# Kernel optimization log

Measured on AMD Instinct MI355X. Metric: run time of the kernel, lower is better.

Reference implementation:

```python
import jax, jax.numpy as jnp
import numpy as np
import math

K = 1.0          # Lorentz curvature parameter (points satisfy -t^2 + |s|^2 = -K)
SQRT_K = 1.0
HEADS = 8
HEAD_DIM = 64
EPS_LN = 1e-5


def add_time(xs):
    # lift space vector onto the hyperboloid: t = sqrt(|s|^2 + K)
    t = jnp.sqrt(jnp.sum(xs * xs, axis=-1, keepdims=True) + K)
    return jnp.concatenate([t, xs], axis=-1)


def logmap0(x):
    t, s = x[..., :1], x[..., 1:]
    d = SQRT_K * jnp.arccosh(jnp.maximum(t / SQRT_K, 1.0))
    sn = jnp.maximum(jnp.linalg.norm(s, axis=-1, keepdims=True), 1e-8)
    return jnp.concatenate([jnp.zeros_like(t), d * s / sn], axis=-1)


def expmap0(u):
    s = u[..., 1:]
    n = jnp.maximum(jnp.linalg.norm(s, axis=-1, keepdims=True), 1e-8)
    t = SQRT_K * jnp.cosh(n / SQRT_K)
    return jnp.concatenate([t, SQRT_K * jnp.sinh(n / SQRT_K) * s / n], axis=-1)


def lorentz_ln(x, g, b):
    # LayerNorm on space coords, then recompute time
    s = x[..., 1:]
    mu = jnp.mean(s, axis=-1, keepdims=True)
    var = jnp.var(s, axis=-1, keepdims=True)
    s = (s - mu) / jnp.sqrt(var + EPS_LN) * g + b
    return add_time(s)


def lfc(x, W, activation=None):
    # LorentzFullyConnected: linear on full input -> space coords, recompute time
    s = x @ W.T
    if activation is not None:
        s = activation(s)
    return add_time(s)


def lfc_heads(x, W):
    b, n, _ = x.shape
    s = (x @ W.T).reshape(b, n, HEADS, HEAD_DIM).transpose(0, 2, 1, 3)
    return add_time(s)  # (b, h, n, head_dim+1), per-head time coordinate


def _mha_haa(x, Wq, Wk, Wv, Wo, temperature, beta_raw, tau_raw, lambda_raw):
    q = lfc_heads(x, Wq)
    k = lfc_heads(x, Wk)
    v = lfc_heads(x, Wv)
    q_t, k_t = q[..., :1], k[..., :1]
    q_s, k_s = q[..., 1:], k[..., 1:]
    # Lorentz inner product <q,k>_L = -t_q t_k + <s_q, s_k>, shape (b,h,n,n)
    inner_QK = -q_t @ jnp.swapaxes(k_t, -1, -2) + q_s @ jnp.swapaxes(k_s, -1, -2)
    inner_OQ = -SQRT_K * q_t                       # (b,h,n,1)
    inner_OK = -SQRT_K * jnp.swapaxes(k_t, -1, -2)  # (b,h,1,n)
    norm_sq_QK = jnp.maximum(inner_QK ** 2 / K - K, 0.0)
    norm_sq_OQ = jnp.maximum(inner_OQ ** 2 / K - K, 0.0)
    numer_Z = inner_OK + inner_QK * inner_OQ / K
    denom_Z = jnp.sqrt(norm_sq_QK * norm_sq_OQ + 0.005 ** 2)
    Z = jnp.clip(numer_Z / denom_Z, -1.0, 1.0)
    c_tilde = jnp.arccosh(jnp.maximum(q_t / SQRT_K, 1.0 + 0.001))
    beta = jax.nn.softplus(beta_raw)
    B = jnp.sqrt(jax.nn.relu(1.0 - (beta / jnp.sinh(c_tilde)) ** 2) + 1e-8)
    lam = jax.nn.softplus(lambda_raw)
    dist_raw = SQRT_K * jnp.arccosh(jnp.maximum(-inner_QK / K, 1.0 + 0.001))
    d_soft = 40.0 * jnp.tanh(dist_raw / 40.0)
    sd = d_soft / 15.0
    H = sd + jax.nn.softplus(-2.0 * sd) - math.log(2.0)
    tau = jax.nn.softplus(tau_raw)
    m = 0.1
    Phi = jax.nn.softplus(B + Z - m) - math.log(1.0 + math.exp(-m))
    score = jax.nn.softmax((-lam * H - tau * Phi) / temperature, axis=-1)
    # Lorentz expmap aggregation: weighted mean in tangent space at origin
    v_tan = logmap0(v)
    mean_tan = (score @ v_tan) / (jnp.sum(score, axis=-1, keepdims=True) + 1e-8)
    attn = expmap0(mean_tan).transpose(0, 2, 1, 3)  # (b,n,h,head_dim+1)
    b_, n_ = attn.shape[:2]
    a_s = attn[..., 1:].reshape(b_, n_, -1)   # (b,n,h*head_dim)
    a_t = attn[..., :1].reshape(b_, n_, -1)   # (b,n,h)
    t2 = jnp.sum(a_t ** 2, axis=-1, keepdims=True) - (HEADS - 1) * K
    attn = jnp.concatenate([jnp.sqrt(jnp.maximum(t2, 1e-8)), a_s], axis=-1)
    return lfc(attn, Wo)


def reference(x, Wq, Wk, Wv, Wo, W1, W2, ln1_g, ln1_b, ln2_g, ln2_b,
              temperature, beta_raw, tau_raw, lambda_raw):
    out = _mha_haa(lorentz_ln(x, ln1_g, ln1_b), Wq, Wk, Wv, Wo,
                   temperature, beta_raw, tau_raw, lambda_raw)
    out_s = out[..., 1:] + x[..., 1:]                 # residual on space coords
    y = lorentz_ln(add_time(out_s), ln2_g, ln2_b)
    h = lfc(y, W1, activation=lambda z: jax.nn.gelu(z, approximate=False))
    h = lfc(h, W2)
    out_s = h[..., 1:] + out_s
    return add_time(out_s)


def setup_inputs() -> dict:
    key = jax.random.key(0)
    ks = jax.random.split(key, 8)
    B, N, D = 2, 1024, 513
    xs = 0.5 * jax.random.normal(ks[0], (B, N, D - 1), dtype=jnp.float32)
    x = add_time(xs)
    sc = 1.0 / math.sqrt(D)
    return {
        "x": x,
        "Wq": sc * jax.random.normal(ks[1], (512, 513), dtype=jnp.float32),
        "Wk": sc * jax.random.normal(ks[2], (512, 513), dtype=jnp.float32),
        "Wv": sc * jax.random.normal(ks[3], (512, 513), dtype=jnp.float32),
        "Wo": sc * jax.random.normal(ks[4], (512, 513), dtype=jnp.float32),
        "W1": sc * jax.random.normal(ks[5], (2048, 513), dtype=jnp.float32),
        "W2": (1.0 / math.sqrt(2049)) * jax.random.normal(ks[6], (512, 2049), dtype=jnp.float32),
        "ln1_g": jnp.ones((512,), jnp.float32),
        "ln1_b": jnp.zeros((512,), jnp.float32),
        "ln2_g": jnp.ones((512,), jnp.float32),
        "ln2_b": jnp.zeros((512,), jnp.float32),
        "temperature": jnp.ones((1,), jnp.float32),
        "beta_raw": jnp.full((1,), math.log(math.e - 1.0), jnp.float32),
        "tau_raw": jnp.full((1,), math.log(math.exp(0.1) - 1.0), jnp.float32),
        "lambda_raw": jnp.full((1,), math.log(math.e - 1.0), jnp.float32),
    }
```

## Files before the change

### kernel.cpp

```cpp
#include <hip/hip_runtime.h>
#include <math.h>

#define DEV static __device__ __forceinline__

typedef __bf16 bf16_t;
typedef __bf16 bf16x8 __attribute__((ext_vector_type(8)));
typedef float f32x4 __attribute__((ext_vector_type(4)));

#define MFMA16(a,b,c) __builtin_amdgcn_mfma_f32_16x16x32_bf16(a,b,c,0,0,0)

DEV float frcp(float x){ return __builtin_amdgcn_rcpf(x); }
DEV float softplus_fast(float x){
  return fmaxf(x, 0.f) + __logf(1.f + __expf(-fabsf(x)));
}
DEV float tanh_fast(float z){
  float e2 = __expf(2.f * z);
  return (e2 - 1.f) * frcp(e2 + 1.f);
}
DEV float gelu_fast(float v){
  float u = 0.7978845608028654f * fmaf(0.044715f * v, v * v, v);
  u = fminf(fmaxf(u, -15.f), 15.f);
  return 0.5f * v * (1.f + tanh_fast(u));
}

DEV void gl_lds16(const void* g, void* l) {
  __builtin_amdgcn_global_load_lds((const __attribute__((address_space(1))) void*)g,
                                   (__attribute__((address_space(3))) void*)l, 16, 0, 0);
}

DEV float waveReduceSum(float v){
  #pragma unroll
  for (int o = 32; o > 0; o >>= 1) v += __shfl_xor(v, o, 64);
  return v;
}
DEV float blockReduceSum(float v, float* sh){
  v = waveReduceSum(v);
  int w = threadIdx.x >> 6;
  int nw = blockDim.x >> 6;
  __syncthreads();
  if ((threadIdx.x & 63) == 0) sh[w] = v;
  __syncthreads();
  float r = sh[0];
  for (int i = 1; i < nw; i++) r += sh[i];
  return r;
}

DEV int2 xcd_swz(int gx, int gy){
  int id = blockIdx.y * gx + blockIdx.x;
  int q = (gx * gy) >> 3;
  int s = (id & 7) * q + (id >> 3);
  int2 r; r.x = s % gx; r.y = s / gx;
  return r;
}

__global__ __launch_bounds__(256) void prep(
    const float* __restrict__ xin,
    const float* __restrict__ g, const float* __restrict__ b,
    const float* __restrict__ Wq, const float* __restrict__ Wk,
    const float* __restrict__ Wv, const float* __restrict__ Wo,
    const float* __restrict__ W1, const float* __restrict__ W2,
    bf16_t* __restrict__ y, float* __restrict__ ty,
    bf16_t* __restrict__ Wqkvb, bf16_t* __restrict__ Wob,
    bf16_t* __restrict__ W1b, bf16_t* __restrict__ W2b,
    float* __restrict__ wqkv0, float* __restrict__ wo0,
    float* __restrict__ w10, float* __restrict__ w20)
{
  int t = threadIdx.x;
  if (blockIdx.x < 2048) {
    __shared__ float sh[8];
    int row = blockIdx.x;
    const float* xr = xin + (long)row * 513 + 1;
    float a0 = xr[t], a1 = xr[t + 256];
    float s  = blockReduceSum(a0 + a1, sh);
    float s2 = blockReduceSum(a0 * a0 + a1 * a1, sh);
    float mu = s * (1.f / 512.f);
    float var = s2 * (1.f / 512.f) - mu * mu;
    float inv = rsqrtf(var + 1e-5f);
    float y0 = (a0 - mu) * inv * g[t] + b[t];
    float y1v = (a1 - mu) * inv * g[t + 256] + b[t + 256];
    float q = blockReduceSum(y0 * y0 + y1v * y1v, sh);
    bf16_t* yr = y + (long)row * 512;
    yr[t] = (bf16_t)y0;
    yr[t + 256] = (bf16_t)y1v;
    if (t == 0) ty[row] = sqrtf(q + 1.f);
    return;
  }
  long i = (long)(blockIdx.x - 2048) * 256 + t;
  if (i < 786432) {
    long r = i >> 9; int c = (int)(i & 511);
    const float* src = (r < 512) ? Wq + r * 513 : (r < 1024) ? Wk + (r - 512) * 513 : Wv + (r - 1024) * 513;
    Wqkvb[i] = (bf16_t)src[c + 1];
  } else if (i < 1048576) {
    long j = i - 786432;
    long r = j >> 9; int c = (int)(j & 511);
    Wob[j] = (bf16_t)Wo[r * 513 + c + 1];
  } else if (i < 2097152) {
    long j = i - 1048576;
    long r = j >> 9; int c = (int)(j & 511);
    W1b[j] = (bf16_t)W1[r * 513 + c + 1];
  } else if (i < 3145728) {
    long j = i - 2097152;
    long r = j >> 11; int c = (int)(j & 2047);
    W2b[j] = (bf16_t)W2[r * 2049 + c + 1];
  } else if (i < 3150336) {
    int j = (int)(i - 3145728);
    if (j < 1536) {
      wqkv0[j] = (j < 512) ? Wq[(long)j * 513] : (j < 1024) ? Wk[(long)(j - 512) * 513] : Wv[(long)(j - 1024) * 513];
    } else if (j < 2048) wo0[j - 1536] = Wo[(long)(j - 1536) * 513];
    else if (j < 4096)  w10[j - 2048] = W1[(long)(j - 2048) * 513];
    else                w20[j - 4096] = W2[(long)(j - 4096) * 2049];
  }
}

__global__ __launch_bounds__(256) void res_ln(
    const float* __restrict__ woA, const float* __restrict__ woB,
    const float* __restrict__ ch2, const float* __restrict__ wo0,
    const float* __restrict__ xin,
    const float* __restrict__ g, const float* __restrict__ b,
    float* __restrict__ outs,
    bf16_t* __restrict__ y, float* __restrict__ ty)
{
  __shared__ float sh[8];
  int row = blockIdx.x;
  int t = threadIdx.x;
  const float* c = ch2 + (long)row * 8;
  float cs = ((c[0] + c[1]) + (c[2] + c[3])) + ((c[4] + c[5]) + (c[6] + c[7]));
  float tattn = sqrtf(fmaxf(cs - 7.f, 1e-8f));
  long i0 = (long)row * 512 + t, i1 = i0 + 256;
  float a0 = woA[i0] + woB[i0] + tattn * wo0[t]       + xin[(long)row * 513 + 1 + t];
  float a1 = woA[i1] + woB[i1] + tattn * wo0[t + 256] + xin[(long)row * 513 + 1 + t + 256];
  outs[i0] = a0;
  outs[i1] = a1;
  float s  = blockReduceSum(a0 + a1, sh);
  float s2 = blockReduceSum(a0 * a0 + a1 * a1, sh);
  float mu = s * (1.f / 512.f);
  float var = s2 * (1.f / 512.f) - mu * mu;
  float inv = rsqrtf(var + 1e-5f);
  float y0 = (a0 - mu) * inv * g[t] + b[t];
  float y1v = (a1 - mu) * inv * g[t + 256] + b[t + 256];
  float q = blockReduceSum(y0 * y0 + y1v * y1v, sh);
  bf16_t* yr = y + (long)row * 512;
  yr[t] = (bf16_t)y0;
  yr[t + 256] = (bf16_t)y1v;
  if (t == 0) ty[row] = sqrtf(q + 1.f);
}

__global__ __launch_bounds__(256) void final_k(
    const float* __restrict__ hA, const float* __restrict__ hB,
    const float* __restrict__ hC, const float* __restrict__ hD,
    const float* __restrict__ th2p, const float* __restrict__ w20,
    const float* __restrict__ outs,
    float* __restrict__ out)
{
  __shared__ float sh[8];
  int row = blockIdx.x;
  int t = threadIdx.x;
  float p = (t < 32) ? th2p[(long)t * 2048 + row] : 0.f;
  float hn = blockReduceSum(p, sh);
  float th = sqrtf(hn + 1.f);
  long i0 = (long)row * 512 + t, i1 = i0 + 256;
  float o0 = (hA[i0] + hB[i0]) + (hC[i0] + hD[i0]) + th * w20[t]       + outs[i0];
  float o1 = (hA[i1] + hB[i1]) + (hC[i1] + hD[i1]) + th * w20[t + 256] + outs[i1];
  float q = blockReduceSum(o0 * o0 + o1 * o1, sh);
  float* yr = out + (long)row * 513;
  yr[1 + t] = o0;
  yr[1 + t + 256] = o1;
  if (t == 0) yr[0] = sqrtf(q + 1.f);
}

__global__ __launch_bounds__(256) void vtan_tr(
    const bf16_t* __restrict__ qkvsb, bf16_t* __restrict__ VTt)
{
  __shared__ bf16_t tile[64 * 72];
  int z = blockIdx.y, b = z >> 3, h = z & 7;
  int n0 = blockIdx.x * 64;
  int t = threadIdx.x;
  int r = t >> 2, c4 = t & 3;
  const bf16_t* vb = qkvsb + ((long)(b * 1024 + n0 + r) * 1536 + 1024 + h * 64 + c4 * 16);
  bf16x8 v0 = *(const bf16x8*)vb;
  bf16x8 v1 = *(const bf16x8*)(vb + 8);
  float ss = 0.f;
  #pragma unroll
  for (int e = 0; e < 8; e++) {
    float f0 = (float)v0[e], f1 = (float)v1[e];
    ss = fmaf(f0, f0, fmaf(f1, f1, ss));
  }
  ss += __shfl_xor(ss, 1, 64);
  ss += __shfl_xor(ss, 2, 64);
  float vT = sqrtf(1.f + ss);
  float sn0 = sqrtf(ss);
  float coef = __logf(vT + sn0) * frcp(fmaxf(sn0, 1e-8f));
  #pragma unroll
  for (int e = 0; e < 8; e++) {
    tile[(c4 * 16 + e) * 72 + r]     = (bf16_t)(coef * (float)v0[e]);
    tile[(c4 * 16 + 8 + e) * 72 + r] = (bf16_t)(coef * (float)v1[e]);
  }
  __syncthreads();
  int d = t >> 2, cc = (t & 3) * 16;
  bf16x8 o0 = *(const bf16x8*)&tile[d * 72 + cc];
  bf16x8 o1 = *(const bf16x8*)&tile[d * 72 + cc + 8];
  bf16_t* dst = VTt + (long)z * 64 * 1024 + (long)d * 1024 + n0 + cc;
  *(bf16x8*)dst = o0;
  *(bf16x8*)(dst + 8) = o1;
}

__global__ __launch_bounds__(256) void attn_fused(
    const bf16_t* __restrict__ qkvsb,
    const bf16_t* __restrict__ VTt,
    const float* __restrict__ qt, const float* __restrict__ kt,
    const float* __restrict__ Bi,
    bf16_t* __restrict__ attnb,
    float* __restrict__ ch2,
    const float* __restrict__ lam_p, const float* __restrict__ tau_p,
    const float* __restrict__ temp_p)
{
  __shared__ bf16_t Ks[64 * 64];
  __shared__ bf16_t Vs[64 * 64];
  __shared__ bf16_t Ps[32 * 72];
  __shared__ float ot[32 * 65];
  __shared__ float sh_qt[32], sh_Bc[32], sh_kt[64], rs[32];

  const int t = threadIdx.x;
  const int w = t >> 6;
  const int lane = t & 63;
  const int lm = lane & 15, lh = lane >> 4;
  int2 sw = xcd_swz(32, 16);
  const int z = sw.y, b = z >> 3, h = z & 7;
  const int n0 = sw.x * 32;
  const int sb = (((lane & 7) ^ (lane >> 3)) << 4);
  const int r8 = lane >> 3;

  float lam = softplus_fast(lam_p[0]);
  float tau = softplus_fast(tau_p[0]);
  float invT = frcp(temp_p[0]);
  float A1 = -lam * invT, A2 = -tau * invT;
  float A2h = 0.5f * A2, K0 = A2 * 0.048750465f;

  if (t < 32) {
    sh_qt[t] = qt[z * 1024 + n0 + t];
    sh_Bc[t] = Bi[z * 1024 + n0 + t] - 0.1f;
    rs[t] = 0.f;
  }

  const bf16_t* qbase = qkvsb + ((long)(b * 1024 + n0) * 1536 + h * 64);
  gl_lds16((const char*)(qbase + (long)(w * 8 + r8) * 1536) + sb, (char*)Ks + w * 1024);
  __syncthreads();
  bf16x8 qf[2][2];
  #pragma unroll
  for (int i = 0; i < 2; i++)
    #pragma unroll
    for (int kk = 0; kk < 2; kk++)
      qf[i][kk] = *(const bf16x8*)&Ks[(i * 16 + lm) * 64 + (((kk * 4 + lh) ^ (lm & 7)) << 3)];

  f32x4 oacc[2] = {};
  float racc[2][4] = {};

  const bf16_t* kbase = qkvsb + ((long)b * 1024 * 1536 + 512 + h * 64);
  const bf16_t* vbase = VTt + (long)z * 64 * 1024;
  const int sl0 = ((lh) ^ (lm & 7)) << 3;
  const int sl1 = ((4 + lh) ^ (lm & 7)) << 3;

  for (int kv = 0; kv < 16; kv++) {
    __syncthreads();
    {
      const bf16_t* kb = kbase + (long)(kv * 64) * 1536;
      gl_lds16((const char*)(kb + (long)(w * 16 + r8) * 1536) + sb,     (char*)Ks + (w * 2) * 1024);
      gl_lds16((const char*)(kb + (long)(w * 16 + 8 + r8) * 1536) + sb, (char*)Ks + (w * 2 + 1) * 1024);
      const bf16_t* vb = vbase + kv * 64;
      gl_lds16((const char*)(vb + (long)(w * 16 + r8) * 1024) + sb,     (char*)Vs + (w * 2) * 1024);
      gl_lds16((const char*)(vb + (long)(w * 16 + 8 + r8) * 1024) + sb, (char*)Vs + (w * 2 + 1) * 1024);
    }
    if (t < 64) sh_kt[t] = kt[z * 1024 + kv * 64 + t];
    __syncthreads();

    f32x4 sacc[2] = {};
    bf16x8 kf0 = *(const bf16x8*)&Ks[(w * 16 + lm) * 64 + sl0];
    bf16x8 kf1 = *(const bf16x8*)&Ks[(w * 16 + lm) * 64 + sl1];
    sacc[0] = MFMA16(qf[0][0], kf0, sacc[0]);
    sacc[0] = MFMA16(qf[0][1], kf1, sacc[0]);
    sacc[1] = MFMA16(qf[1][0], kf0, sacc[1]);
    sacc[1] = MFMA16(qf[1][1], kf1, sacc[1]);

    float ktv = sh_kt[w * 16 + lm];
    #pragma unroll
    for (int i = 0; i < 2; i++) {
      #pragma unroll
      for (int q = 0; q < 4; q++) {
        int r = i * 16 + lh * 4 + q;
        float qtv = sh_qt[r], Bc = sh_Bc[r];
        float nOQ = fmaf(qtv, qtv, -1.f);
        float inner = fmaf(-qtv, ktv, sacc[i][q]);
        float nQK = fmaxf(fmaf(inner, inner, -1.f), 0.f);
        float ri = __builtin_amdgcn_rsqf(fmaf(nQK, nOQ, 2.5e-5f));
        float zr = fmaf(inner, qtv, ktv) * ri;
        float Zc = fminf(fmaxf(-zr, -1.f), 1.f);
        float xx = fmaxf(-inner, 1.001f);
        float u = fmaf(__log2f(xx), 0.01732868f, 0.01732868f);
        float p = fminf(u * u, 0.09f);
        float H = p * fmaf(p, -6.584f, 3.5556f);
        float a = Zc + Bc;
        float a2 = a * a;
        float lc = a2 * fmaf(a2, fmaf(a2, 0.00034722f, -0.0052083f), 0.125f);
        float lgt = fmaf(A1, H, fmaf(A2, lc, fmaf(A2h, a, K0)));
        float e = __expf(lgt);
        Ps[r * 72 + w * 16 + lm] = (bf16_t)e;
        racc[i][q] += e;
      }
    }
    __syncthreads();

    bf16x8 va0 = *(const bf16x8*)&Vs[(w * 16 + lm) * 64 + sl0];
    bf16x8 va1 = *(const bf16x8*)&Vs[(w * 16 + lm) * 64 + sl1];
    bf16x8 pb00 = *(const bf16x8*)&Ps[lm * 72 + lh * 8];
    bf16x8 pb01 = *(const bf16x8*)&Ps[lm * 72 + 32 + lh * 8];
    bf16x8 pb10 = *(const bf16x8*)&Ps[(16 + lm) * 72 + lh * 8];
    bf16x8 pb11 = *(const bf16x8*)&Ps[(16 + lm) * 72 + 32 + lh * 8];
    oacc[0] = MFMA16(va0, pb00, oacc[0]);
    oacc[0] = MFMA16(va1, pb01, oacc[0]);
    oacc[1] = MFMA16(va0, pb10, oacc[1]);
    oacc[1] = MFMA16(va1, pb11, oacc[1]);
  }

  #pragma unroll
  for (int i = 0; i < 2; i++)
    #pragma unroll
    for (int q = 0; q < 4; q++) {
      float v = racc[i][q];
      v += __shfl_xor(v, 1, 64);
      v += __shfl_xor(v, 2, 64);
      v += __shfl_xor(v, 4, 64);
      v += __shfl_xor(v, 8, 64);
      if (lm == 0) atomicAdd(&rs[i * 16 + lh * 4 + q], v);
    }

  #pragma unroll
  for (int j = 0; j < 2; j++)
    #pragma unroll
    for (int q = 0; q < 4; q++)
      ot[(j * 16 + lm) * 65 + w * 16 + lh * 4 + q] = oacc[j][q];
  __syncthreads();

  int r = t >> 3, c0 = (t & 7) * 8;
  float inv = frcp(rs[r] * (1.f + 1e-8f));
  float v[8];
  float ss = 0.f;
  #pragma unroll
  for (int e = 0; e < 8; e++) {
    v[e] = ot[r * 65 + c0 + e] * inv;
    ss = fmaf(v[e], v[e], ss);
  }
  ss += __shfl_xor(ss, 1, 64);
  ss += __shfl_xor(ss, 2, 64);
  ss += __shfl_xor(ss, 4, 64);
  float nn = fmaxf(sqrtf(ss), 1e-8f);
  float e_ = __expf(nn), ei = frcp(e_);
  float coef = 0.5f * (e_ - ei) * frcp(nn);
  bf16x8 ov;
  #pragma unroll
  for (int e = 0; e < 8; e++) ov[e] = (bf16_t)(coef * v[e]);
  *(bf16x8*)(attnb + (long)(b * 1024 + n0 + r) * 512 + h * 64 + c0) = ov;
  if (c0 == 0) {
    float ch = 0.5f * (e_ + ei);
    ch2[(long)(b * 1024 + n0 + r) * 8 + h] = ch * ch;
  }
}

template<int ACTF, int STATS>
DEV void gemm_rep_body(
    const bf16_t* __restrict__ Ag, int lda,
    const bf16_t* __restrict__ Bg, int ldb,
    bf16_t* __restrict__ Cg, int ldc, int K,
    const float* __restrict__ trow, const float* __restrict__ w0,
    float* __restrict__ s0, float* __restrict__ s1, float* __restrict__ s2,
    const float* __restrict__ beta_p,
    int bx, int by)
{
  __shared__ char smem[24576];
  __shared__ float sh_t[128];
  bf16_t* As = (bf16_t*)smem;
  bf16_t* Bs = (bf16_t*)(smem + 16384);
  const int t = threadIdx.x;
  const int wid = t >> 6, lane = t & 63;
  const int lm = lane & 15, lh = lane >> 4;
  const int bm = bx * 128;
  const int bn = by * 64;
  const int wm = (wid >> 1) * 64;
  const int wn = (wid & 1) * 32;
  const int sb = (((lane & 7) ^ (lane >> 3)) << 4);
  const int r8 = lane >> 3;
  f32x4 acc[4][2] = {};

  if (t < 128) sh_t[t] = trow[bm + t];
  float w0c[2] = { w0[bn + wn + lm], w0[bn + wn + 16 + lm] };

  for (int kk = 0; kk < K; kk += 64) {
    __syncthreads();
    #pragma unroll
    for (int r = 0; r < 4; r++) {
      int chunk = wid * 4 + r;
      gl_lds16((const char*)(Ag + (long)(bm + chunk * 8 + r8) * lda + kk) + sb,
               smem + chunk * 1024);
    }
    #pragma unroll
    for (int r = 0; r < 2; r++) {
      int chunk = wid * 2 + r;
      gl_lds16((const char*)(Bg + (long)(bn + chunk * 8 + r8) * ldb + kk) + sb,
               smem + 16384 + chunk * 1024);
    }
    __syncthreads();
    #pragma unroll
    for (int k2 = 0; k2 < 2; k2++) {
      const int sl = (((k2 * 4 + lh) ^ (lm & 7)) << 3);
      bf16x8 af[4], bfr[2];
      #pragma unroll
      for (int i = 0; i < 4; i++) af[i] = *(const bf16x8*)&As[(wm + i * 16 + lm) * 64 + sl];
      #pragma unroll
      for (int j = 0; j < 2; j++) bfr[j] = *(const bf16x8*)&Bs[(wn + j * 16 + lm) * 64 + sl];
      #pragma unroll
      for (int i = 0; i < 4; i++)
        #pragma unroll
        for (int j = 0; j < 2; j++)
          acc[i][j] = MFMA16(af[i], bfr[j], acc[i][j]);
    }
  }

  __syncthreads();
  bf16_t* rep = (bf16_t*)smem;
  #pragma unroll
  for (int i = 0; i < 4; i++) {
    #pragma unroll
    for (int q = 0; q < 4; q++) {
      int r = wm + i * 16 + lh * 4 + q;
      #pragma unroll
      for (int j = 0; j < 2; j++) {
        float v = acc[i][j][q] + sh_t[r] * w0c[j];
        rep[r * 64 + wn + j * 16 + lm] = (bf16_t)(ACTF == 0 ? gelu_fast(v) : v);
      }
    }
  }
  __syncthreads();

  #pragma unroll
  for (int rd = 0; rd < 4; rd++) {
    int off = rd * 4096 + t * 16;
    int lr = off >> 7;
    int lc = (off & 127) >> 1;
    bf16x8 vv = *(const bf16x8*)(smem + off);
    *(bf16x8*)(Cg + (long)(bm + lr) * ldc + bn + lc) = vv;
  }

  if constexpr (STATS != 0) {
    int rr = t >> 1, half = t & 1;
    const bf16_t* rp = rep + rr * 64 + half * 32;
    float s = 0.f;
    #pragma unroll
    for (int c = 0; c < 4; c++) {
      bf16x8 vv = *(const bf16x8*)(rp + c * 8);
      #pragma unroll
      for (int e = 0; e < 8; e++) { float f = (float)vv[e]; s = fmaf(f, f, s); }
    }
    s += __shfl_xor(s, 1, 64);
    if (half == 0) {
      if constexpr (STATS == 2) {
        s0[(long)(bn >> 6) * 2048 + bm + rr] = s;
      } else {
        int bnh = bn >> 6;
        if (bnh < 16) {
          int grow = bm + rr, bloc = grow >> 10, n = grow & 1023;
          if (bnh < 8) {
            int zz = bloc * 8 + bnh;
            float qT = sqrtf(1.f + s);
            s0[zz * 1024 + n] = qT;
            float beta = softplus_fast(beta_p[0]);
            float xq = fmaxf(qT, 1.001f);
            float sh_ = sqrtf(fmaxf(xq * xq - 1.f, 0.f));
            float rr0 = beta * frcp(sh_);
            s2[zz * 1024 + n] = sqrtf(fmaxf(1.f - rr0 * rr0, 0.f) + 1e-8f);
          } else {
            int zz = bloc * 8 + (bnh - 8);
            s1[zz * 1024 + n] = sqrtf(1.f + s);
          }
        }
      }
    }
  }
}

DEV void gemm_f32_body(
    const bf16_t* __restrict__ Ag, int lda,
    const bf16_t* __restrict__ Bg, int ldb,
    float* __restrict__ Cg, int ldc,
    int k0, int k1, int bx, int by)
{
  __shared__ bf16_t As[64 * 64];
  __shared__ bf16_t Bs[64 * 64];
  const int t = threadIdx.x;
  const int wid = t >> 6, lane = t & 63;
  const int lm = lane & 15, lh = lane >> 4;
  const int bm = bx * 64;
  const int bn = by * 64;
  const int wm = (wid >> 1) * 32;
  const int wn = (wid & 1) * 32;
  const int sb = (((lane & 7) ^ (lane >> 3)) << 4);
  const int r8 = lane >> 3;
  f32x4 acc[2][2] = {};

  for (int kk = k0; kk < k1; kk += 64) {
    __syncthreads();
    #pragma unroll
    for (int r = 0; r < 2; r++) {
      int chunk = wid * 2 + r;
      gl_lds16((const char*)(Ag + (long)(bm + chunk * 8 + r8) * lda + kk) + sb,
               (char*)As + chunk * 1024);
      gl_lds16((const char*)(Bg + (long)(bn + chunk * 8 + r8) * ldb + kk) + sb,
               (char*)Bs + chunk * 1024);
    }
    __syncthreads();
    #pragma unroll
    for (int k2 = 0; k2 < 2; k2++) {
      const int sl = (((k2 * 4 + lh) ^ (lm & 7)) << 3);
      bf16x8 af[2], bfr[2];
      #pragma unroll
      for (int i = 0; i < 2; i++) af[i] = *(const bf16x8*)&As[(wm + i * 16 + lm) * 64 + sl];
      #pragma unroll
      for (int j = 0; j < 2; j++) bfr[j] = *(const bf16x8*)&Bs[(wn + j * 16 + lm) * 64 + sl];
      #pragma unroll
      for (int i = 0; i < 2; i++)
        #pragma unroll
        for (int j = 0; j < 2; j++)
          acc[i][j] = MFMA16(af[i], bfr[j], acc[i][j]);
    }
  }

  #pragma unroll
  for (int i = 0; i < 2; i++) {
    #pragma unroll
    for (int q = 0; q < 4; q++) {
      long row = bm + wm + i * 16 + lh * 4 + q;
      #pragma unroll
      for (int j = 0; j < 2; j++)
        Cg[row * ldc + bn + wn + j * 16 + lm] = acc[i][j][q];
    }
  }
}

__global__ __launch_bounds__(256) void gemm_qkv(const bf16_t* A, int lda, const bf16_t* B, int ldb,
                                                bf16_t* C, int ldc, int K,
                                                const float* trow, const float* w0,
                                                float* qt, float* kt, float* Bi, const float* beta){
  int2 sw = xcd_swz(16, 24);
  gemm_rep_body<2, 1>(A, lda, B, ldb, C, ldc, K, trow, w0, qt, kt, Bi, beta, sw.x, sw.y);
}
__global__ __launch_bounds__(256) void gemm_f1(const bf16_t* A, int lda, const bf16_t* B, int ldb,
                                               bf16_t* C, int ldc, int K,
                                               const float* trow, const float* w0,
                                               float* th2p){
  int2 sw = xcd_swz(16, 32);
  gemm_rep_body<0, 2>(A, lda, B, ldb, C, ldc, K, trow, w0, th2p, nullptr, nullptr, nullptr, sw.x, sw.y);
}
__global__ __launch_bounds__(256) void gemm_wo(const bf16_t* A, int lda, const bf16_t* B, int ldb,
                                               float* C, int ldc, int K){
  int2 sw = xcd_swz(32, 8);
  int k0 = blockIdx.z * (K >> 1);
  gemm_f32_body(A, lda, B, ldb, C + (long)blockIdx.z * 2048 * ldc, ldc,
                k0, k0 + (K >> 1), sw.x, sw.y);
}
__global__ __launch_bounds__(256) void gemm_f2(const bf16_t* A, int lda, const bf16_t* B, int ldb,
                                               float* C, int ldc, int K){
  int2 sw = xcd_swz(32, 8);
  int k0 = blockIdx.z * (K >> 2);
  gemm_f32_body(A, lda, B, ldb, C + (long)blockIdx.z * 2048 * ldc, ldc,
                k0, k0 + (K >> 2), sw.x, sw.y);
}

extern "C" void kernel_launch(void* const* d_in, const int* in_sizes, int n_in,
                              void* d_out, int out_size, void* d_ws, size_t ws_size,
                              hipStream_t stream) {
  const float* x    = (const float*)d_in[0];
  const float* Wq   = (const float*)d_in[1];
  const float* Wk   = (const float*)d_in[2];
  const float* Wv   = (const float*)d_in[3];
  const float* Wo   = (const float*)d_in[4];
  const float* W1   = (const float*)d_in[5];
  const float* W2   = (const float*)d_in[6];
  const float* g1   = (const float*)d_in[7];
  const float* b1   = (const float*)d_in[8];
  const float* g2   = (const float*)d_in[9];
  const float* b2   = (const float*)d_in[10];
  const float* temp = (const float*)d_in[11];
  const float* beta = (const float*)d_in[12];
  const float* tau  = (const float*)d_in[13];
  const float* lam  = (const float*)d_in[14];

  char* W = (char*)d_ws;
  bf16_t* Wqkvb = (bf16_t*)(W + 0);
  bf16_t* Wob   = (bf16_t*)(W + 1572864);
  bf16_t* W1b   = (bf16_t*)(W + 2097152);
  bf16_t* W2b   = (bf16_t*)(W + 4194304);
  float*  wqkv0 = (float*) (W + 6291456);
  float*  wo0   = (float*) (W + 6297600);
  float*  w10   = (float*) (W + 6299648);
  float*  w20   = (float*) (W + 6307840);
  bf16_t* y1b   = (bf16_t*)(W + 6309888);
  float*  ty1   = (float*) (W + 8407040);
  bf16_t* qkvsb = (bf16_t*)(W + 8415232);
  float*  qt    = (float*) (W + 14706688);
  float*  kt    = (float*) (W + 14772224);
  float*  Bi    = (float*) (W + 14837760);
  bf16_t* VTt   = (bf16_t*)(W + 14903296);
  float*  ch2   = (float*) (W + 17000448);
  bf16_t* attnb = (bf16_t*)(W + 17065984);
  float*  tmpA  = (float*) (W + 19163136);
  float*  outs  = (float*) (W + 35940352);
  bf16_t* y2b   = (bf16_t*)(W + 40134656);
  float*  ty2   = (float*) (W + 42231808);
  bf16_t* hb    = (bf16_t*)(W + 42240000);
  float*  th2p  = (float*) (W + 50628608);
  float*  tmpB  = tmpA + 1048576;
  float*  tmpC  = tmpA + 2097152;
  float*  tmpD  = tmpA + 3145728;

  prep<<<14354, 256, 0, stream>>>(x, g1, b1, Wq, Wk, Wv, Wo, W1, W2,
                                  y1b, ty1, Wqkvb, Wob, W1b, W2b, wqkv0, wo0, w10, w20);

  gemm_qkv<<<dim3(16,24,1),256,0,stream>>>(y1b, 512, Wqkvb, 512, qkvsb, 1536, 512,
                                           ty1, wqkv0, qt, kt, Bi, beta);

  vtan_tr<<<dim3(16,16,1),256,0,stream>>>(qkvsb, VTt);

  attn_fused<<<dim3(32,16,1),256,0,stream>>>(qkvsb, VTt, qt, kt, Bi, attnb, ch2, lam, tau, temp);

  gemm_wo<<<dim3(32,8,2),256,0,stream>>>(attnb, 512, Wob, 512, tmpA, 512, 512);

  res_ln<<<2048, 256, 0, stream>>>(tmpA, tmpB, ch2, wo0, x, g2, b2, outs, y2b, ty2);

  gemm_f1<<<dim3(16,32,1),256,0,stream>>>(y2b, 512, W1b, 512, hb, 2048, 512, ty2, w10, th2p);

  gemm_f2<<<dim3(32,8,4),256,0,stream>>>(hb, 2048, W2b, 2048, tmpA, 512, 2048);

  final_k<<<2048, 256, 0, stream>>>(tmpA, tmpB, tmpC, tmpD, th2p, w20, outs, (float*)d_out);
}
```

Measured before the change: 101.7 us.

## Fuse V logmap-transpose into QKV GEMM epilogue and drop XCD swizzle

The separate vtan_tr kernel is removed. The QKV GEMM blocks that produce V columns (blockIdx.y >= 16) now compute the per-row logmap coefficient from the bf16 tile in shared memory and write the scaled, transposed V directly to VTt, saving a launch and a re-read of V from global memory. Separately, the XCD block-index swizzle is removed from all GEMM and attention kernels in favour of plain blockIdx mapping, which may change L2 locality across XCDs. A side effect is that V-column blocks no longer write V into qkvsb, so attention must read V only through VTt.

```diff
diff --git a/kernel.cpp b/kernel.cpp
--- a/kernel.cpp
+++ b/kernel.cpp
@@ -42,14 +42,6 @@
   __syncthreads();
   float r = sh[0];
   for (int i = 1; i < nw; i++) r += sh[i];
-  return r;
-}
-
-DEV int2 xcd_swz(int gx, int gy){
-  int id = blockIdx.y * gx + blockIdx.x;
-  int q = (gx * gy) >> 3;
-  int s = (id & 7) * q + (id >> 3);
-  int2 r; r.x = s % gx; r.y = s / gx;
   return r;
 }
 
@@ -168,42 +160,6 @@
   if (t == 0) yr[0] = sqrtf(q + 1.f);
 }
 
-__global__ __launch_bounds__(256) void vtan_tr(
-    const bf16_t* __restrict__ qkvsb, bf16_t* __restrict__ VTt)
-{
-  __shared__ bf16_t tile[64 * 72];
-  int z = blockIdx.y, b = z >> 3, h = z & 7;
-  int n0 = blockIdx.x * 64;
-  int t = threadIdx.x;
-  int r = t >> 2, c4 = t & 3;
-  const bf16_t* vb = qkvsb + ((long)(b * 1024 + n0 + r) * 1536 + 1024 + h * 64 + c4 * 16);
-  bf16x8 v0 = *(const bf16x8*)vb;
-  bf16x8 v1 = *(const bf16x8*)(vb + 8);
-  float ss = 0.f;
-  #pragma unroll
-  for (int e = 0; e < 8; e++) {
-    float f0 = (float)v0[e], f1 = (float)v1[e];
-    ss = fmaf(f0, f0, fmaf(f1, f1, ss));
-  }
-  ss += __shfl_xor(ss, 1, 64);
-  ss += __shfl_xor(ss, 2, 64);
-  float vT = sqrtf(1.f + ss);
-  float sn0 = sqrtf(ss);
-  float coef = __logf(vT + sn0) * frcp(fmaxf(sn0, 1e-8f));
-  #pragma unroll
-  for (int e = 0; e < 8; e++) {
-    tile[(c4 * 16 + e) * 72 + r]     = (bf16_t)(coef * (float)v0[e]);
-    tile[(c4 * 16 + 8 + e) * 72 + r] = (bf16_t)(coef * (float)v1[e]);
-  }
-  __syncthreads();
-  int d = t >> 2, cc = (t & 3) * 16;
-  bf16x8 o0 = *(const bf16x8*)&tile[d * 72 + cc];
-  bf16x8 o1 = *(const bf16x8*)&tile[d * 72 + cc + 8];
-  bf16_t* dst = VTt + (long)z * 64 * 1024 + (long)d * 1024 + n0 + cc;
-  *(bf16x8*)dst = o0;
-  *(bf16x8*)(dst + 8) = o1;
-}
-
 __global__ __launch_bounds__(256) void attn_fused(
     const bf16_t* __restrict__ qkvsb,
     const bf16_t* __restrict__ VTt,
@@ -224,9 +180,8 @@
   const int w = t >> 6;
   const int lane = t & 63;
   const int lm = lane & 15, lh = lane >> 4;
-  int2 sw = xcd_swz(32, 16);
-  const int z = sw.y, b = z >> 3, h = z & 7;
-  const int n0 = sw.x * 32;
+  const int z = blockIdx.y, b = z >> 3, h = z & 7;
+  const int n0 = blockIdx.x * 32;
   const int sb = (((lane & 7) ^ (lane >> 3)) << 4);
   const int r8 = lane >> 3;
 
@@ -373,17 +328,18 @@
     const float* __restrict__ trow, const float* __restrict__ w0,
     float* __restrict__ s0, float* __restrict__ s1, float* __restrict__ s2,
     const float* __restrict__ beta_p,
-    int bx, int by)
+    bf16_t* __restrict__ vtt)
 {
   __shared__ char smem[24576];
   __shared__ float sh_t[128];
+  __shared__ float shc[128];
   bf16_t* As = (bf16_t*)smem;
   bf16_t* Bs = (bf16_t*)(smem + 16384);
   const int t = threadIdx.x;
   const int wid = t >> 6, lane = t & 63;
   const int lm = lane & 15, lh = lane >> 4;
-  const int bm = bx * 128;
-  const int bn = by * 64;
+  const int bm = blockIdx.x * 128;
+  const int bn = blockIdx.y * 64;
   const int wm = (wid >> 1) * 64;
   const int wn = (wid & 1) * 32;
   const int sb = (((lane & 7) ^ (lane >> 3)) << 4);
@@ -425,6 +381,61 @@
   }
 
   __syncthreads();
+
+  if (STATS == 1 && blockIdx.y >= 16) {
+    bf16_t* repv = (bf16_t*)smem;
+    #pragma unroll
+    for (int i = 0; i < 4; i++) {
+      #pragma unroll
+      for (int q = 0; q < 4; q++) {
+        int r = wm + i * 16 + lh * 4 + q;
+        #pragma unroll
+        for (int j = 0; j < 2; j++) {
+          float v = acc[i][j][q] + sh_t[r] * w0c[j];
+          repv[r * 68 + wn + j * 16 + lm] = (bf16_t)v;
+        }
+      }
+    }
+    __syncthreads();
+    {
+      int rr = t >> 1, half = t & 1;
+      const bf16_t* rp = repv + rr * 68 + half * 32;
+      float s = 0.f;
+      #pragma unroll
+      for (int c = 0; c < 4; c++) {
+        bf16x8 vv = *(const bf16x8*)(rp + c * 8);
+        #pragma unroll
+        for (int e = 0; e < 8; e++) { float f = (float)vv[e]; s = fmaf(f, f, s); }
+      }
+      s += __shfl_xor(s, 1, 64);
+      if (half == 0) {
+        float sn0 = sqrtf(s);
+        float vT = sqrtf(1.f + s);
+        shc[rr] = __logf(vT + sn0) * frcp(fmaxf(sn0, 1e-8f));
+      }
+    }
+    __syncthreads();
+    {
+      int zz = (bm >> 10) * 8 + (blockIdx.y - 16);
+      int nb = bm & 1023;
+      int dbase = (t >> 4) * 4;
+      int m = t & 15;
+      bf16_t* dstz = vtt + (long)zz * 65536;
+      #pragma unroll
+      for (int p = 0; p < 4; p++) {
+        int d = dbase + p;
+        bf16x8 ov;
+        #pragma unroll
+        for (int e = 0; e < 8; e++) {
+          int n = m * 8 + e;
+          ov[e] = (bf16_t)((float)repv[n * 68 + d] * shc[n]);
+        }
+        *(bf16x8*)(dstz + (long)d * 1024 + nb + m * 8) = ov;
+      }
+    }
+    return;
+  }
+
   bf16_t* rep = (bf16_t*)smem;
   #pragma unroll
   for (int i = 0; i < 4; i++) {
@@ -462,24 +473,22 @@
     s += __shfl_xor(s, 1, 64);
     if (half == 0) {
       if constexpr (STATS == 2) {
-        s0[(long)(bn >> 6) * 2048 + bm + rr] = s;
+        s0[(long)blockIdx.y * 2048 + bm + rr] = s;
       } else {
-        int bnh = bn >> 6;
-        if (bnh < 16) {
-          int grow = bm + rr, bloc = grow >> 10, n = grow & 1023;
-          if (bnh < 8) {
-            int zz = bloc * 8 + bnh;
-            float qT = sqrtf(1.f + s);
-            s0[zz * 1024 + n] = qT;
-            float beta = softplus_fast(beta_p[0]);
-            float xq = fmaxf(qT, 1.001f);
-            float sh_ = sqrtf(fmaxf(xq * xq - 1.f, 0.f));
-            float rr0 = beta * frcp(sh_);
-            s2[zz * 1024 + n] = sqrtf(fmaxf(1.f - rr0 * rr0, 0.f) + 1e-8f);
-          } else {
-            int zz = bloc * 8 + (bnh - 8);
-            s1[zz * 1024 + n] = sqrtf(1.f + s);
-          }
+        int bnh = blockIdx.y;
+        int grow = bm + rr, bloc = grow >> 10, n = grow & 1023;
+        if (bnh < 8) {
+          int zz = bloc * 8 + bnh;
+          float qT = sqrtf(1.f + s);
+          s0[zz * 1024 + n] = qT;
+          float beta = softplus_fast(beta_p[0]);
+          float xq = fmaxf(qT, 1.001f);
+          float sh_ = sqrtf(fmaxf(xq * xq - 1.f, 0.f));
+          float rr0 = beta * frcp(sh_);
+          s2[zz * 1024 + n] = sqrtf(fmaxf(1.f - rr0 * rr0, 0.f) + 1e-8f);
+        } else {
+          int zz = bloc * 8 + (bnh - 8);
+          s1[zz * 1024 + n] = sqrtf(1.f + s);
         }
       }
     }
@@ -490,15 +499,15 @@
     const bf16_t* __restrict__ Ag, int lda,
     const bf16_t* __restrict__ Bg, int ldb,
     float* __restrict__ Cg, int ldc,
-    int k0, int k1, int bx, int by)
+    int k0, int k1)
 {
   __shared__ bf16_t As[64 * 64];
   __shared__ bf16_t Bs[64 * 64];
   const int t = threadIdx.x;
   const int wid = t >> 6, lane = t & 63;
   const int lm = lane & 15, lh = lane >> 4;
-  const int bm = bx * 64;
-  const int bn = by * 64;
+  const int bm = blockIdx.x * 64;
+  const int bn = blockIdx.y * 64;
   const int wm = (wid >> 1) * 32;
   const int wn = (wid & 1) * 32;
   const int sb = (((lane & 7) ^ (lane >> 3)) << 4);
@@ -547,30 +556,25 @@
 __global__ __launch_bounds__(256) void gemm_qkv(const bf16_t* A, int lda, const bf16_t* B, int ldb,
                                                 bf16_t* C, int ldc, int K,
                                                 const float* trow, const float* w0,
-                                                float* qt, float* kt, float* Bi, const float* beta){
-  int2 sw = xcd_swz(16, 24);
-  gemm_rep_body<2, 1>(A, lda, B, ldb, C, ldc, K, trow, w0, qt, kt, Bi, beta, sw.x, sw.y);
+                                                float* qt, float* kt, float* Bi, const float* beta,
+                                                bf16_t* vtt){
+  gemm_rep_body<2, 1>(A, lda, B, ldb, C, ldc, K, trow, w0, qt, kt, Bi, beta, vtt);
 }
 __global__ __launch_bounds__(256) void gemm_f1(const bf16_t* A, int lda, const bf16_t* B, int ldb,
                                                bf16_t* C, int ldc, int K,
                                                const float* trow, const float* w0,
                                                float* th2p){
-  int2 sw = xcd_swz(16, 32);
-  gemm_rep_body<0, 2>(A, lda, B, ldb, C, ldc, K, trow, w0, th2p, nullptr, nullptr, nullptr, sw.x, sw.y);
+  gemm_rep_body<0, 2>(A, lda, B, ldb, C, ldc, K, trow, w0, th2p, nullptr, nullptr, nullptr, nullptr);
 }
 __global__ __launch_bounds__(256) void gemm_wo(const bf16_t* A, int lda, const bf16_t* B, int ldb,
                                                float* C, int ldc, int K){
-  int2 sw = xcd_swz(32, 8);
   int k0 = blockIdx.z * (K >> 1);
-  gemm_f32_body(A, lda, B, ldb, C + (long)blockIdx.z * 2048 * ldc, ldc,
-                k0, k0 + (K >> 1), sw.x, sw.y);
+  gemm_f32_body(A, lda, B, ldb, C + (long)blockIdx.z * 2048 * ldc, ldc, k0, k0 + (K >> 1));
 }
 __global__ __launch_bounds__(256) void gemm_f2(const bf16_t* A, int lda, const bf16_t* B, int ldb,
                                                float* C, int ldc, int K){
-  int2 sw = xcd_swz(32, 8);
   int k0 = blockIdx.z * (K >> 2);
-  gemm_f32_body(A, lda, B, ldb, C + (long)blockIdx.z * 2048 * ldc, ldc,
-                k0, k0 + (K >> 2), sw.x, sw.y);
+  gemm_f32_body(A, lda, B, ldb, C + (long)blockIdx.z * 2048 * ldc, ldc, k0, k0 + (K >> 2));
 }
 
 extern "C" void kernel_launch(void* const* d_in, const int* in_sizes, int n_in,
@@ -624,9 +628,7 @@
                                   y1b, ty1, Wqkvb, Wob, W1b, W2b, wqkv0, wo0, w10, w20);
 
   gemm_qkv<<<dim3(16,24,1),256,0,stream>>>(y1b, 512, Wqkvb, 512, qkvsb, 1536, 512,
-                                           ty1, wqkv0, qt, kt, Bi, beta);
-
-  vtan_tr<<<dim3(16,16,1),256,0,stream>>>(qkvsb, VTt);
+                                           ty1, wqkv0, qt, kt, Bi, beta, VTt);
 
   attn_fused<<<dim3(32,16,1),256,0,stream>>>(qkvsb, VTt, qt, kt, Bi, attnb, ch2, lam, tau, temp);
 
```

Measured after the change: 96.51 us. 5.1% less time.
